# Kernel tuning notes

Hardware: AMD Instinct MI355X
Metric: run time of the kernel (lower is better)

## Reference

```python
import jax, jax.numpy as jnp
import numpy as np

NC = 80        # number of classes
CONF = 0.25    # confidence threshold
RATIO = 0.1    # top-k fraction


def setup_inputs() -> dict:
    key = jax.random.key(0)
    N = 2097152
    data = jax.random.normal(key, (1, N, 4 + NC), dtype=jnp.float32)
    return {"data": data}


def reference(data):
    pred = data[0]                      # [N, 4+nc]
    cls_logits = pred[:, -NC:]          # [N, nc]
    boxes = pred[:, :4]                 # [N, 4]
    scores = jnp.max(cls_logits, axis=1)  # class_id is None -> max over classes
    n = scores.shape[0]
    k = max(1, min(n, int(np.ceil(n * float(RATIO)))))  # static k
    vals, idx = jax.lax.top_k(scores, k)   # [k], [k]
    mask = vals >= CONF                     # [k] bool
    # torch returns 0.0 when mask is empty; masked sums naturally give 0 then.
    loss = jnp.sum(jnp.where(mask, vals, 0.0))
    # output_type == 'all' -> add gathered box sums for masked top-k indices
    loss = loss + jnp.sum(jnp.where(mask[:, None], boxes[idx], 0.0))
    return loss
```

## Files before the change

### kernel.cpp

```cpp
#include <hip/hip_runtime.h>
#include <stdint.h>
#include <math.h>

#define ROWLEN 84
#define F4PR 21
#define CANDCAP (1u << 20)

__device__ __forceinline__ uint32_t map_f(float f) {
    uint32_t u = __float_as_uint(f);
    return (u & 0x80000000u) ? ~u : (u | 0x80000000u);
}
__device__ __forceinline__ float unmap_f(uint32_t u) {
    uint32_t b = (u & 0x80000000u) ? (u & 0x7FFFFFFFu) : ~u;
    return __uint_as_float(b);
}

__device__ void find_parallel(const uint32_t* hist, int nbins, uint32_t target,
                              uint32_t* s, uint32_t* sc2, uint32_t* outBin, uint32_t* outAbove) {
    int tid = threadIdx.x;
    int chunks = nbins / 256;
    int base = tid * chunks;
    uint32_t part = 0;
    for (int i = 0; i < chunks; ++i) part += hist[base + i];
    s[tid] = part;
    __syncthreads();
    for (int off = 1; off < 256; off <<= 1) {
        uint32_t v = (tid + off < 256) ? s[tid + off] : 0u;
        __syncthreads();
        s[tid] += v;
        __syncthreads();
    }
    uint32_t above_next = (tid < 255) ? s[tid + 1] : 0u;
    bool mine = (s[tid] >= target) && (above_next < target);
    if (mine) { sc2[0] = (uint32_t)tid; sc2[1] = above_next; }
    __syncthreads();
    uint32_t c = sc2[0], above = sc2[1];
    if (tid == 0) {
        uint32_t acc = above;
        int b = (int)c * chunks + chunks - 1;
        for (;; --b) {
            uint32_t hb = hist[b];
            if (acc + hb >= target) break;
            acc += hb;
        }
        sc2[0] = (uint32_t)b;
        sc2[1] = acc;
    }
    __syncthreads();
    *outBin = sc2[0];
    *outAbove = sc2[1];
}

__global__ __launch_bounds__(256) void k_score_hist(const float* __restrict__ pred,
                                                    uint32_t* __restrict__ scores,
                                                    uint32_t* __restrict__ gH1,
                                                    uint32_t* __restrict__ candCnt,
                                                    float* __restrict__ out, int n) {
    __shared__ uint32_t h[1024];
    int tid = threadIdx.x;
    if (blockIdx.x == 0 && tid == 0) { *out = 0.f; *candCnt = 0u; }
    for (int i = tid; i < 1024; i += 256) h[i] = 0;
    __syncthreads();
    const float4* pf4 = (const float4*)pred;
    size_t total_f4 = (size_t)n * F4PR;
    int lane = tid & 63;
    int wv = (blockIdx.x * 256 + tid) >> 6;
    int nw = gridDim.x * 4;
    int g = lane / 21;
    int rel = lane - g * 21;
    bool lv = (lane < 63);
    int ntrip = (n + 2) / 3;
    const int OFFS[5] = {10, 5, 3, 2, 1};
    for (int t0 = wv * 2; t0 < ntrip; t0 += nw * 2) {
        float mA = -INFINITY, mB = -INFINITY;
        size_t iA = (size_t)t0 * 63 + lane;
        size_t iB = iA + 63;
        if (lv && rel != 0 && iA < total_f4) {
            float4 v = pf4[iA];
            mA = fmaxf(fmaxf(v.x, v.y), fmaxf(v.z, v.w));
        }
        if (lv && rel != 0 && iB < total_f4) {
            float4 v = pf4[iB];
            mB = fmaxf(fmaxf(v.x, v.y), fmaxf(v.z, v.w));
        }
#pragma unroll
        for (int k = 0; k < 5; ++k) {
            int off = OFFS[k];
            float oA = __shfl(mA, lane + off);
            float oB = __shfl(mB, lane + off);
            if (rel + off <= 20) { mA = fmaxf(mA, oA); mB = fmaxf(mB, oB); }
        }
        if (rel == 1) {
            int rA = t0 * 3 + g;
            if (rA < n) {
                uint32_t u = map_f(mA);
                scores[rA] = u;
                atomicAdd(&h[u >> 22], 1u);
            }
            int rB = rA + 3;
            if (rB < n) {
                uint32_t u = map_f(mB);
                scores[rB] = u;
                atomicAdd(&h[u >> 22], 1u);
            }
        }
    }
    __syncthreads();
    for (int i = tid; i < 1024; i += 256)
        if (h[i]) atomicAdd(&gH1[i], h[i]);
}

__global__ void k_hist2f(const uint32_t* __restrict__ scores, const uint32_t* __restrict__ gH1,
                         uint32_t* __restrict__ gH2, uint32_t* __restrict__ sres,
                         int n, uint32_t K) {
    __shared__ uint32_t h[2048];
    __shared__ uint32_t s[256];
    __shared__ uint32_t sc2[2];
    for (int i = threadIdx.x; i < 2048; i += 256) h[i] = 0;
    uint32_t bin1, chi1;
    find_parallel(gH1, 1024, K, s, sc2, &bin1, &chi1);
    if (blockIdx.x == 0 && threadIdx.x == 0) { sres[0] = bin1; sres[1] = chi1; }
    int gid = blockIdx.x * 256 + threadIdx.x;
    int stride = gridDim.x * 256;
    const uint4* s4 = (const uint4*)scores;
    int n4 = n >> 2;
    for (int i = gid; i < n4; i += stride) {
        uint4 uu = s4[i];
        if ((uu.x >> 22) == bin1) atomicAdd(&h[(uu.x >> 11) & 0x7FFu], 1u);
        if ((uu.y >> 22) == bin1) atomicAdd(&h[(uu.y >> 11) & 0x7FFu], 1u);
        if ((uu.z >> 22) == bin1) atomicAdd(&h[(uu.z >> 11) & 0x7FFu], 1u);
        if ((uu.w >> 22) == bin1) atomicAdd(&h[(uu.w >> 11) & 0x7FFu], 1u);
    }
    for (int r = n4 * 4 + gid; r < n; r += stride) {
        uint32_t u = scores[r];
        if ((u >> 22) == bin1) atomicAdd(&h[(u >> 11) & 0x7FFu], 1u);
    }
    __syncthreads();
    for (int i = threadIdx.x; i < 2048; i += 256)
        if (h[i]) atomicAdd(&gH2[i], h[i]);
}

__global__ void k_select2(const float* __restrict__ pred, const uint32_t* __restrict__ scores,
                          const uint32_t* __restrict__ gH2, uint32_t* __restrict__ sres,
                          uint32_t* __restrict__ candCnt, uint2* __restrict__ candBuf,
                          float* __restrict__ out, int n, uint32_t K) {
    __shared__ uint32_t s[256];
    __shared__ uint32_t sc2[2];
    __shared__ float wsum[4];
    uint32_t bin1 = sres[0], chi1 = sres[1];
    uint32_t bin2, chi2;
    find_parallel(gH2, 2048, K - chi1, s, sc2, &bin2, &chi2);
    uint32_t t21 = (bin1 << 11) | bin2;
    uint32_t chiTot = chi1 + chi2;
    if (blockIdx.x == 0 && threadIdx.x == 0) {
        sres[2] = t21; sres[3] = chiTot; sres[4] = K - chiTot;
    }
    const uint32_t u_conf = 0xBE800000u;
    const uint32_t CONF21 = u_conf >> 11;
    bool tcut = (t21 >= CONF21);
    float lsum = 0.f;
    int gid = blockIdx.x * 256 + threadIdx.x;
    int stride = gridDim.x * 256;
    const uint4* s4 = (const uint4*)scores;
    int n4 = n >> 2;
    for (int i = gid; i < n4; i += stride) {
        uint4 uu = s4[i];
#pragma unroll
        for (int j = 0; j < 4; ++j) {
            uint32_t u = (j == 0) ? uu.x : (j == 1) ? uu.y : (j == 2) ? uu.z : uu.w;
            int r = i * 4 + j;
            bool sel = tcut ? ((u >> 11) > t21) : (u >= u_conf);
            if (sel) {
                float4 b = *(const float4*)(pred + (size_t)r * ROWLEN);
                lsum += unmap_f(u) + b.x + b.y + b.z + b.w;
            }
            if (tcut && (u >> 11) == t21) {
                uint32_t pos = atomicAdd(candCnt, 1u);
                if (pos < CANDCAP) candBuf[pos] = make_uint2((uint32_t)r, u);
            }
        }
    }
    for (int r = n4 * 4 + gid; r < n; r += stride) {
        uint32_t u = scores[r];
        bool sel = tcut ? ((u >> 11) > t21) : (u >= u_conf);
        if (sel) {
            float4 b = *(const float4*)(pred + (size_t)r * ROWLEN);
            lsum += unmap_f(u) + b.x + b.y + b.z + b.w;
        }
        if (tcut && (u >> 11) == t21) {
            uint32_t pos = atomicAdd(candCnt, 1u);
            if (pos < CANDCAP) candBuf[pos] = make_uint2((uint32_t)r, u);
        }
    }
    for (int off = 32; off; off >>= 1) lsum += __shfl_down(lsum, off);
    int wid = threadIdx.x >> 6, lane = threadIdx.x & 63;
    if (lane == 0) wsum[wid] = lsum;
    __syncthreads();
    if (threadIdx.x == 0) atomicAdd(out, wsum[0] + wsum[1] + wsum[2] + wsum[3]);
}

__global__ void k_final(const float* __restrict__ pred, const uint32_t* __restrict__ sres,
                        const uint32_t* __restrict__ candCnt, const uint2* __restrict__ candBuf,
                        float* __restrict__ out) {
    __shared__ uint32_t h[2048];
    __shared__ uint32_t s[256];
    __shared__ uint32_t sc2[2];
    __shared__ float wsum[4];
    __shared__ uint32_t tb[1024];
    __shared__ uint32_t tc;
    uint32_t t21 = sres[2];
    const uint32_t u_conf = 0xBE800000u;
    const uint32_t CONF21 = u_conf >> 11;
    if (t21 < CONF21) return;
    uint32_t mprime = sres[4];
    uint32_t cc = *candCnt;
    if (cc > CANDCAP) cc = CANDCAP;
    int tid = threadIdx.x;
    for (int i = tid; i < 2048; i += 256) h[i] = 0;
    if (tid == 0) tc = 0;
    __syncthreads();
    for (uint32_t i = tid; i < cc; i += 256) atomicAdd(&h[candBuf[i].y & 0x7FFu], 1u);
    __syncthreads();
    uint32_t bin3, chi3;
    find_parallel(h, 2048, mprime, s, sc2, &bin3, &chi3);
    uint32_t t_u = (t21 << 11) | bin3;
    uint32_t mt = mprime - chi3;
    float lsum = 0.f;
    for (uint32_t i = tid; i < cc; i += 256) {
        uint2 c = candBuf[i];
        uint32_t low = c.y & 0x7FFu;
        if (low > bin3) {
            float4 b = *(const float4*)(pred + (size_t)c.x * ROWLEN);
            lsum += unmap_f(c.y) + b.x + b.y + b.z + b.w;
        } else if (low == bin3) {
            uint32_t p = atomicAdd(&tc, 1u);
            if (p < 1024) tb[p] = c.x;
        }
    }
    __syncthreads();
    uint32_t tcnt = tc;
    if (tcnt > 1024) tcnt = 1024;
    if (mt >= tcnt) {
        for (uint32_t i = tid; i < tcnt; i += 256) {
            float4 b = *(const float4*)(pred + (size_t)tb[i] * ROWLEN);
            lsum += b.x + b.y + b.z + b.w;
        }
    } else {
        for (uint32_t i = tid; i < tcnt; i += 256) {
            uint32_t ri = tb[i];
            uint32_t rank = 0;
            for (uint32_t j = 0; j < tcnt; ++j) rank += (tb[j] < ri) ? 1u : 0u;
            if (rank < mt) {
                float4 b = *(const float4*)(pred + (size_t)ri * ROWLEN);
                lsum += b.x + b.y + b.z + b.w;
            }
        }
    }
    for (int off = 32; off; off >>= 1) lsum += __shfl_down(lsum, off);
    int wid = tid >> 6, lane = tid & 63;
    if (lane == 0) wsum[wid] = lsum;
    __syncthreads();
    if (tid == 0)
        atomicAdd(out, wsum[0] + wsum[1] + wsum[2] + wsum[3] + (float)mt * unmap_f(t_u));
}

extern "C" void kernel_launch(void* const* d_in, const int* in_sizes, int n_in,
                              void* d_out, int out_size, void* d_ws, size_t ws_size,
                              hipStream_t stream) {
    const float* pred = (const float*)d_in[0];
    int n = in_sizes[0] / ROWLEN;
    double kd = ceil((double)n * 0.1);
    long kk = (long)kd;
    if (kk < 1) kk = 1;
    if (kk > n) kk = n;
    uint32_t K = (uint32_t)kk;

    uint32_t* ws32 = (uint32_t*)d_ws;
    uint32_t* scores = ws32;
    uint32_t* gH1 = ws32 + n;
    uint32_t* gH2 = gH1 + 1024;
    uint32_t* candCnt = gH2 + 2048;
    uint32_t* sres = candCnt + 16;
    uint2* candBuf = (uint2*)(sres + 16);
    float* out = (float*)d_out;

    hipMemsetAsync(gH1, 0, (1024 + 2048) * sizeof(uint32_t), stream);

    k_score_hist<<<2048, 256, 0, stream>>>(pred, scores, gH1, candCnt, out, n);
    k_hist2f<<<1024, 256, 0, stream>>>(scores, gH1, gH2, sres, n, K);
    k_select2<<<2048, 256, 0, stream>>>(pred, scores, gH2, sres, candCnt, candBuf, out, n, K);
    k_final<<<1, 256, 0, stream>>>(pred, sres, candCnt, candBuf, out);
}
```

Baseline: 209.4 us.

## Stage score rows through LDS tiles and fold final pass into last select block

The score kernel now loads 128-row tiles with fully coalesced float4 reads into shared memory, masking the box lanes, and reduces each row's class maxima from LDS instead of using cross-lane shuffles over 63-lane groups. The single-block final kernel is removed: k_select2 uses a global done counter so the last finishing block performs the candidate refinement, which saves one launch. Candidate entries become 64-bit atomic stores so the last block reads them coherently. The cost is higher LDS use per block, which may lower occupancy, plus an extra atomic per block.

```diff
diff --git a/kernel.cpp b/kernel.cpp
--- a/kernel.cpp
+++ b/kernel.cpp
@@ -4,7 +4,9 @@
 
 #define ROWLEN 84
 #define F4PR 21
-#define CANDCAP (1u << 20)
+#define RPB 128
+#define F4PT (RPB * F4PR)
+#define CANDCAP (1u << 21)
 
 __device__ __forceinline__ uint32_t map_f(float f) {
     uint32_t u = __float_as_uint(f);
@@ -54,55 +56,61 @@
 __global__ __launch_bounds__(256) void k_score_hist(const float* __restrict__ pred,
                                                     uint32_t* __restrict__ scores,
                                                     uint32_t* __restrict__ gH1,
-                                                    uint32_t* __restrict__ candCnt,
                                                     float* __restrict__ out, int n) {
+    __shared__ float pm[F4PT];
     __shared__ uint32_t h[1024];
     int tid = threadIdx.x;
-    if (blockIdx.x == 0 && tid == 0) { *out = 0.f; *candCnt = 0u; }
+    if (blockIdx.x == 0 && tid == 0) *out = 0.f;
     for (int i = tid; i < 1024; i += 256) h[i] = 0;
-    __syncthreads();
+    uint32_t tid21 = (uint32_t)tid % 21u;
     const float4* pf4 = (const float4*)pred;
     size_t total_f4 = (size_t)n * F4PR;
+    int ntiles = (n + RPB - 1) / RPB;
     int lane = tid & 63;
-    int wv = (blockIdx.x * 256 + tid) >> 6;
-    int nw = gridDim.x * 4;
-    int g = lane / 21;
-    int rel = lane - g * 21;
-    bool lv = (lane < 63);
-    int ntrip = (n + 2) / 3;
-    const int OFFS[5] = {10, 5, 3, 2, 1};
-    for (int t0 = wv * 2; t0 < ntrip; t0 += nw * 2) {
-        float mA = -INFINITY, mB = -INFINITY;
-        size_t iA = (size_t)t0 * 63 + lane;
-        size_t iB = iA + 63;
-        if (lv && rel != 0 && iA < total_f4) {
-            float4 v = pf4[iA];
-            mA = fmaxf(fmaxf(v.x, v.y), fmaxf(v.z, v.w));
-        }
-        if (lv && rel != 0 && iB < total_f4) {
-            float4 v = pf4[iB];
-            mB = fmaxf(fmaxf(v.x, v.y), fmaxf(v.z, v.w));
-        }
+    int rloc = (tid >> 6) * 32 + (lane >> 1);
+    int par = lane & 1;
+    for (int tile = blockIdx.x; tile < ntiles; tile += gridDim.x) {
+        __syncthreads();
+        size_t gbase = (size_t)tile * F4PT;
+        int row0 = tile * RPB;
+        if (row0 + RPB <= n) {
 #pragma unroll
-        for (int k = 0; k < 5; ++k) {
-            int off = OFFS[k];
-            float oA = __shfl(mA, lane + off);
-            float oB = __shfl(mB, lane + off);
-            if (rel + off <= 20) { mA = fmaxf(mA, oA); mB = fmaxf(mB, oB); }
-        }
-        if (rel == 1) {
-            int rA = t0 * 3 + g;
-            if (rA < n) {
-                uint32_t u = map_f(mA);
-                scores[rA] = u;
-                atomicAdd(&h[u >> 22], 1u);
-            }
-            int rB = rA + 3;
-            if (rB < n) {
-                uint32_t u = map_f(mB);
-                scores[rB] = u;
-                atomicAdd(&h[u >> 22], 1u);
-            }
+            for (int it = 0; it < 11; ++it) {
+                int l = it * 256 + tid;
+                if (l < F4PT) {
+                    const uint32_t BP = (21u - (4u * (uint32_t)it) % 21u) % 21u;
+                    float4 v = pf4[gbase + l];
+                    float m = fmaxf(fmaxf(v.x, v.y), fmaxf(v.z, v.w));
+                    pm[l] = (tid21 == BP) ? -INFINITY : m;
+                }
+            }
+        } else {
+#pragma unroll
+            for (int it = 0; it < 11; ++it) {
+                int l = it * 256 + tid;
+                if (l < F4PT) {
+                    const uint32_t BP = (21u - (4u * (uint32_t)it) % 21u) % 21u;
+                    size_t g = gbase + l;
+                    float m = -INFINITY;
+                    if (g < total_f4 && tid21 != BP) {
+                        float4 v = pf4[g];
+                        m = fmaxf(fmaxf(v.x, v.y), fmaxf(v.z, v.w));
+                    }
+                    pm[l] = m;
+                }
+            }
+        }
+        __syncthreads();
+        const float* q = pm + rloc * F4PR + 1 + par * 10;
+        float m = q[0];
+#pragma unroll
+        for (int j = 1; j < 10; ++j) m = fmaxf(m, q[j]);
+        m = fmaxf(m, __shfl_xor(m, 1));
+        int row = row0 + rloc;
+        if (par == 0 && row < n) {
+            uint32_t u = map_f(m);
+            scores[row] = u;
+            atomicAdd(&h[u >> 22], 1u);
         }
     }
     __syncthreads();
@@ -141,25 +149,29 @@
 }
 
 __global__ void k_select2(const float* __restrict__ pred, const uint32_t* __restrict__ scores,
-                          const uint32_t* __restrict__ gH2, uint32_t* __restrict__ sres,
-                          uint32_t* __restrict__ candCnt, uint2* __restrict__ candBuf,
-                          float* __restrict__ out, int n, uint32_t K) {
+                          const uint32_t* __restrict__ gH2, const uint32_t* __restrict__ sres,
+                          uint32_t* __restrict__ candCnt, unsigned long long* __restrict__ candBuf,
+                          uint32_t* __restrict__ done, float* __restrict__ out,
+                          int n, uint32_t K) {
+    __shared__ uint32_t h[2048];
     __shared__ uint32_t s[256];
     __shared__ uint32_t sc2[2];
     __shared__ float wsum[4];
+    __shared__ uint32_t tb[1024];
+    __shared__ uint32_t tc;
+    __shared__ uint32_t s_last;
+    int tid = threadIdx.x;
     uint32_t bin1 = sres[0], chi1 = sres[1];
     uint32_t bin2, chi2;
     find_parallel(gH2, 2048, K - chi1, s, sc2, &bin2, &chi2);
     uint32_t t21 = (bin1 << 11) | bin2;
     uint32_t chiTot = chi1 + chi2;
-    if (blockIdx.x == 0 && threadIdx.x == 0) {
-        sres[2] = t21; sres[3] = chiTot; sres[4] = K - chiTot;
-    }
+    uint32_t mprime = K - chiTot;
     const uint32_t u_conf = 0xBE800000u;
     const uint32_t CONF21 = u_conf >> 11;
     bool tcut = (t21 >= CONF21);
     float lsum = 0.f;
-    int gid = blockIdx.x * 256 + threadIdx.x;
+    int gid = blockIdx.x * 256 + tid;
     int stride = gridDim.x * 256;
     const uint4* s4 = (const uint4*)scores;
     int n4 = n >> 2;
@@ -176,7 +188,11 @@
             }
             if (tcut && (u >> 11) == t21) {
                 uint32_t pos = atomicAdd(candCnt, 1u);
-                if (pos < CANDCAP) candBuf[pos] = make_uint2((uint32_t)r, u);
+                if (pos < CANDCAP) {
+                    unsigned long long v = ((unsigned long long)u << 32) | (uint32_t)r;
+                    __hip_atomic_store(&candBuf[pos], v, __ATOMIC_RELAXED,
+                                       __HIP_MEMORY_SCOPE_AGENT);
+                }
             }
         }
     }
@@ -189,52 +205,53 @@
         }
         if (tcut && (u >> 11) == t21) {
             uint32_t pos = atomicAdd(candCnt, 1u);
-            if (pos < CANDCAP) candBuf[pos] = make_uint2((uint32_t)r, u);
+            if (pos < CANDCAP) {
+                unsigned long long v = ((unsigned long long)u << 32) | (uint32_t)r;
+                __hip_atomic_store(&candBuf[pos], v, __ATOMIC_RELAXED, __HIP_MEMORY_SCOPE_AGENT);
+            }
         }
     }
     for (int off = 32; off; off >>= 1) lsum += __shfl_down(lsum, off);
-    int wid = threadIdx.x >> 6, lane = threadIdx.x & 63;
+    int wid = tid >> 6, lane = tid & 63;
     if (lane == 0) wsum[wid] = lsum;
     __syncthreads();
-    if (threadIdx.x == 0) atomicAdd(out, wsum[0] + wsum[1] + wsum[2] + wsum[3]);
-}
-
-__global__ void k_final(const float* __restrict__ pred, const uint32_t* __restrict__ sres,
-                        const uint32_t* __restrict__ candCnt, const uint2* __restrict__ candBuf,
-                        float* __restrict__ out) {
-    __shared__ uint32_t h[2048];
-    __shared__ uint32_t s[256];
-    __shared__ uint32_t sc2[2];
-    __shared__ float wsum[4];
-    __shared__ uint32_t tb[1024];
-    __shared__ uint32_t tc;
-    uint32_t t21 = sres[2];
-    const uint32_t u_conf = 0xBE800000u;
-    const uint32_t CONF21 = u_conf >> 11;
-    if (t21 < CONF21) return;
-    uint32_t mprime = sres[4];
-    uint32_t cc = *candCnt;
+    if (tid == 0) {
+        atomicAdd(out, wsum[0] + wsum[1] + wsum[2] + wsum[3]);
+        uint32_t prev = __hip_atomic_fetch_add(done, 1u, __ATOMIC_ACQ_REL,
+                                               __HIP_MEMORY_SCOPE_AGENT);
+        s_last = (prev == gridDim.x - 1) ? 1u : 0u;
+    }
+    __syncthreads();
+    if (!s_last || !tcut) return;
+
+    uint32_t cc = __hip_atomic_load(candCnt, __ATOMIC_RELAXED, __HIP_MEMORY_SCOPE_AGENT);
     if (cc > CANDCAP) cc = CANDCAP;
-    int tid = threadIdx.x;
     for (int i = tid; i < 2048; i += 256) h[i] = 0;
     if (tid == 0) tc = 0;
     __syncthreads();
-    for (uint32_t i = tid; i < cc; i += 256) atomicAdd(&h[candBuf[i].y & 0x7FFu], 1u);
+    for (uint32_t i = tid; i < cc; i += 256) {
+        unsigned long long v = __hip_atomic_load(&candBuf[i], __ATOMIC_RELAXED,
+                                                 __HIP_MEMORY_SCOPE_AGENT);
+        atomicAdd(&h[(uint32_t)(v >> 32) & 0x7FFu], 1u);
+    }
     __syncthreads();
     uint32_t bin3, chi3;
     find_parallel(h, 2048, mprime, s, sc2, &bin3, &chi3);
     uint32_t t_u = (t21 << 11) | bin3;
     uint32_t mt = mprime - chi3;
-    float lsum = 0.f;
+    float fsum = 0.f;
     for (uint32_t i = tid; i < cc; i += 256) {
-        uint2 c = candBuf[i];
-        uint32_t low = c.y & 0x7FFu;
+        unsigned long long v = __hip_atomic_load(&candBuf[i], __ATOMIC_RELAXED,
+                                                 __HIP_MEMORY_SCOPE_AGENT);
+        uint32_t key = (uint32_t)(v >> 32);
+        uint32_t r = (uint32_t)v;
+        uint32_t low = key & 0x7FFu;
         if (low > bin3) {
-            float4 b = *(const float4*)(pred + (size_t)c.x * ROWLEN);
-            lsum += unmap_f(c.y) + b.x + b.y + b.z + b.w;
+            float4 b = *(const float4*)(pred + (size_t)r * ROWLEN);
+            fsum += unmap_f(key) + b.x + b.y + b.z + b.w;
         } else if (low == bin3) {
             uint32_t p = atomicAdd(&tc, 1u);
-            if (p < 1024) tb[p] = c.x;
+            if (p < 1024) tb[p] = r;
         }
     }
     __syncthreads();
@@ -243,7 +260,7 @@
     if (mt >= tcnt) {
         for (uint32_t i = tid; i < tcnt; i += 256) {
             float4 b = *(const float4*)(pred + (size_t)tb[i] * ROWLEN);
-            lsum += b.x + b.y + b.z + b.w;
+            fsum += b.x + b.y + b.z + b.w;
         }
     } else {
         for (uint32_t i = tid; i < tcnt; i += 256) {
@@ -252,13 +269,12 @@
             for (uint32_t j = 0; j < tcnt; ++j) rank += (tb[j] < ri) ? 1u : 0u;
             if (rank < mt) {
                 float4 b = *(const float4*)(pred + (size_t)ri * ROWLEN);
-                lsum += b.x + b.y + b.z + b.w;
-            }
-        }
-    }
-    for (int off = 32; off; off >>= 1) lsum += __shfl_down(lsum, off);
-    int wid = tid >> 6, lane = tid & 63;
-    if (lane == 0) wsum[wid] = lsum;
+                fsum += b.x + b.y + b.z + b.w;
+            }
+        }
+    }
+    for (int off = 32; off; off >>= 1) fsum += __shfl_down(fsum, off);
+    if (lane == 0) wsum[wid] = fsum;
     __syncthreads();
     if (tid == 0)
         atomicAdd(out, wsum[0] + wsum[1] + wsum[2] + wsum[3] + (float)mt * unmap_f(t_u));
@@ -280,14 +296,15 @@
     uint32_t* gH1 = ws32 + n;
     uint32_t* gH2 = gH1 + 1024;
     uint32_t* candCnt = gH2 + 2048;
-    uint32_t* sres = candCnt + 16;
-    uint2* candBuf = (uint2*)(sres + 16);
+    uint32_t* done = candCnt + 16;
+    uint32_t* sres = done + 16;
+    unsigned long long* candBuf = (unsigned long long*)(sres + 16);
     float* out = (float*)d_out;
 
-    hipMemsetAsync(gH1, 0, (1024 + 2048) * sizeof(uint32_t), stream);
-
-    k_score_hist<<<2048, 256, 0, stream>>>(pred, scores, gH1, candCnt, out, n);
+    hipMemsetAsync(gH1, 0, (1024 + 2048 + 16 + 16) * sizeof(uint32_t), stream);
+
+    k_score_hist<<<2048, 256, 0, stream>>>(pred, scores, gH1, out, n);
     k_hist2f<<<1024, 256, 0, stream>>>(scores, gH1, gH2, sres, n, K);
-    k_select2<<<2048, 256, 0, stream>>>(pred, scores, gH2, sres, candCnt, candBuf, out, n, K);
-    k_final<<<1, 256, 0, stream>>>(pred, sres, candCnt, candBuf, out);
-}
+    k_select2<<<2048, 256, 0, stream>>>(pred, scores, gH2, sres, candCnt, candBuf,
+                                        done, out, n, K);
+}
```

New measurement: 232.5 us. +11.0%, slower.
